# Kernel optimization log

Measured on AMD Instinct MI355X. Metric: run time of the kernel, lower is better.

## Reference

```python
import jax, jax.numpy as jnp
import numpy as np

N_NODES = 100000
N_HYPEREDGES = 20000
NNZ = 600000
D = 128


def setup_inputs() -> dict:
    key = jax.random.key(0)
    k = jax.random.split(key, 6)
    s = 1.0 / np.sqrt(D)
    x = jax.random.normal(k[0], (N_NODES, D), jnp.float32)
    node_idx = jax.random.randint(k[1], (NNZ,), 0, N_NODES, dtype=jnp.int64 if jax.config.jax_enable_x64 else jnp.int32)
    edge_idx = jax.random.randint(k[2], (NNZ,), 0, N_HYPEREDGES, dtype=jnp.int64 if jax.config.jax_enable_x64 else jnp.int32)
    conv_W = jax.random.uniform(k[3], (D, D), jnp.float32, -s, s)
    conv_b = jnp.zeros((D,), jnp.float32)
    res_W = jax.random.uniform(k[4], (D, D), jnp.float32, -s, s)
    res_b = jax.random.uniform(k[5], (D,), jnp.float32, -s, s)
    return {"x": x, "node_idx": node_idx, "edge_idx": edge_idx,
            "conv_W": conv_W, "conv_b": conv_b, "res_W": res_W, "res_b": res_b}


def hypergraph_conv(x, node_idx, edge_idx, W, b):
    # PyG HypergraphConv (no attention, unit hyperedge weights):
    #   out = D^{-1} H B^{-1} H^T (x W) + b
    y = x @ W                                                      # [N, D]
    ones = jnp.ones(node_idx.shape, dtype=y.dtype)
    deg_n = jax.ops.segment_sum(ones, node_idx, num_segments=N_NODES)        # node degree
    deg_e = jax.ops.segment_sum(ones, edge_idx, num_segments=N_HYPEREDGES)   # hyperedge size
    inv_n = jnp.where(deg_n > 0, 1.0 / deg_n, 0.0)
    inv_e = jnp.where(deg_e > 0, 1.0 / deg_e, 0.0)
    # node -> hyperedge aggregation, normalized by B^{-1}
    e_feat = jax.ops.segment_sum(y[node_idx], edge_idx, num_segments=N_HYPEREDGES)
    e_feat = e_feat * inv_e[:, None]                               # [E, D]
    # hyperedge -> node aggregation, normalized by D^{-1}
    out = jax.ops.segment_sum(e_feat[edge_idx], node_idx, num_segments=N_NODES)
    out = out * inv_n[:, None]                                     # [N, D]
    return out + b


def reference(x, node_idx, edge_idx, conv_W, conv_b, res_W, res_b):
    h = hypergraph_conv(x, node_idx, edge_idx, conv_W, conv_b)     # layer_num = 1
    return (x @ res_W + res_b) + h                                 # residual Linear + conv out
```

## Files before the change

kernel.cpp:

```cpp
#include <hip/hip_runtime.h>

#define N_NODES 100000
#define N_EDGES 20000
#define NNZ_C   600000
#define D 128

typedef short bf16x8 __attribute__((ext_vector_type(8)));
typedef float f32x4  __attribute__((ext_vector_type(4)));

__device__ __forceinline__ unsigned short f2bf(float f) {
    unsigned int u = __float_as_uint(f);
    u = (u + 0x7fffu + ((u >> 16) & 1u)) >> 16;
    return (unsigned short)u;
}
__device__ __forceinline__ float bf2f(unsigned short h) {
    return __uint_as_float((unsigned int)h << 16);
}
__device__ __forceinline__ unsigned int pk_trunc(float lo, float hi) {
    return __builtin_amdgcn_perm(__float_as_uint(hi), __float_as_uint(lo),
                                 0x07060302);
}

#define CH 4096
#define NCHUNK 147
#define CONVB 256
#define WBLK 8
#define EBW 16
#define NBE 1250
#define ECAP 768
#define NBW 64
#define NBN 1563
#define NCAP 640
#define PADI 32
#define GCUR_INTS ((NBE + NBN) * PADI)
#define TAGSH 21
#define PKMASK 0x1FFFFF

#define GT 64
#define XPAD 136

__global__ __launch_bounds__(512) void fused_bin_conv(
    const float* __restrict__ x,
    const int* __restrict__ nidx, const int* __restrict__ eidx,
    const float* __restrict__ cW, const float* __restrict__ rW,
    unsigned short* __restrict__ xb,
    unsigned short* __restrict__ wtc, unsigned short* __restrict__ wtr,
    int* __restrict__ bucket_e, int* __restrict__ bucket_n,
    int* __restrict__ gcur_e, int* __restrict__ gcur_n) {
    __shared__ int srt[CH];
    __shared__ int cnt[NBN], lbase[NBN], gbase[NBN], cur[NBN];
    const int bid = blockIdx.x;
    const int tid = threadIdx.x;

    if (bid >= NCHUNK + CONVB) {
        const int t0 = (bid - NCHUNK - CONVB) * 4096;
        for (int i = tid; i < 4096; i += 512) {
            const int t = t0 + i;
            const int m = t >> 14, idx = t & 16383;
            const int f = idx & 127, k = idx >> 7;
            const float* src = m ? rW : cW;
            unsigned short* dst = m ? wtr : wtc;
            dst[f * D + k] = f2bf(src[k * D + f]);
        }
        return;
    }
    if (bid >= NCHUNK) {
        const int total8 = N_NODES * D / 8;
        for (int g = (bid - NCHUNK) * 512 + tid; g < total8;
             g += CONVB * 512) {
            const float4 a = *(const float4*)(x + (size_t)g * 8);
            const float4 c = *(const float4*)(x + (size_t)g * 8 + 4);
            uint4 v;
            v.x = pk_trunc(a.x, a.y);
            v.y = pk_trunc(a.z, a.w);
            v.z = pk_trunc(c.x, c.y);
            v.w = pk_trunc(c.z, c.w);
            *(uint4*)(xb + (size_t)g * 8) = v;
        }
        return;
    }

    const int j0 = bid * CH;
    const int jn = (j0 + CH < NNZ_C) ? CH : NNZ_C - j0;
#pragma unroll
    for (int s = 0; s < 2; ++s) {
        const int nb = s ? NBN : NBE;
        int* gc = s ? gcur_n : gcur_e;
        int* dst = s ? bucket_n : bucket_e;
        const int cap = s ? NCAP : ECAP;
        for (int i = tid; i < nb; i += 512) cnt[i] = 0;
        __syncthreads();
        for (int i = tid; i < jn; i += 512) {
            const int id = s ? nidx[j0 + i] : eidx[j0 + i];
            atomicAdd(&cnt[s ? (id >> 6) : (id >> 4)], 1);
        }
        __syncthreads();
        if (tid < 64) {
            int loc[25];
            int ssum = 0;
            const int k0 = tid * 25;
#pragma unroll
            for (int k = 0; k < 25; ++k) {
                const int idx = k0 + k;
                loc[k] = ssum;
                if (idx < nb) ssum += cnt[idx];
            }
            int v = ssum;
#pragma unroll
            for (int off = 1; off < 64; off <<= 1) {
                const int t = __shfl_up(v, off);
                if (tid >= off) v += t;
            }
            const int base = v - ssum;
#pragma unroll
            for (int k = 0; k < 25; ++k) {
                const int idx = k0 + k;
                if (idx < nb) {
                    lbase[idx] = base + loc[k];
                    cur[idx] = base + loc[k];
                }
            }
        }
        __syncthreads();
        for (int i = tid; i < nb; i += 512)
            gbase[i] = cnt[i] ? atomicAdd(&gc[i * PADI], cnt[i]) : 0;
        __syncthreads();
        for (int i = tid; i < jn; i += 512) {
            const int e = eidx[j0 + i], n = nidx[j0 + i];
            const int b = s ? (n >> 6) : (e >> 4);
            const unsigned pk = s ? (unsigned)(((n & 63) << 15) | e)
                                  : (unsigned)(((e & 15) << 17) | n);
            const int pos = atomicAdd(&cur[b], 1);
            srt[pos] = (int)(pk | ((unsigned)b << TAGSH));
        }
        __syncthreads();
        for (int i = tid; i < jn; i += 512) {
            const unsigned v = (unsigned)srt[i];
            const int b = (int)(v >> TAGSH);
            const int o2 = gbase[b] + (i - lbase[b]);
            if (o2 < cap) dst[b * cap + o2] = (int)(v & PKMASK);
        }
        __syncthreads();
    }
}

__global__ __launch_bounds__(256) void edge_mean(
    const int* __restrict__ bucket_e, const int* __restrict__ gcur_e,
    const unsigned short* __restrict__ xb, unsigned short* __restrict__ sb) {
    __shared__ int srt[ECAP];
    __shared__ int cnt[EBW + 1];
    __shared__ int cur[EBW];
    const int tid = threadIdx.x;
    const int b = blockIdx.x;
    int W = gcur_e[b * PADI];
    if (W > ECAP) W = ECAP;
    if (tid <= EBW) cnt[tid] = 0;
    __syncthreads();
    const int* src = bucket_e + b * ECAP;
    for (int i = tid; i < W; i += 256)
        atomicAdd(&cnt[src[i] >> 17], 1);
    __syncthreads();
    if (tid < EBW) {
        const int c = cnt[tid];
        int v = c;
#pragma unroll
        for (int off = 1; off < EBW; off <<= 1) {
            const int t = __shfl_up(v, off);
            if (tid >= off) v += t;
        }
        cnt[tid] = v - c;
        cur[tid] = v - c;
        if (tid == EBW - 1) cnt[EBW] = v;
    }
    __syncthreads();
    for (int i = tid; i < W; i += 256) {
        const int p = src[i];
        const int pos = atomicAdd(&cur[p >> 17], 1);
        srt[pos] = p & 0x1FFFF;
    }
    __syncthreads();

    const int g = tid >> 4;
    const int l = tid & 15;
    const int beg = cnt[g], end = cnt[g + 1];
    float acc[8] = {};
    int j = beg;
    for (; j + 8 <= end; j += 8) {
        bf16x8 p[8];
#pragma unroll
        for (int q = 0; q < 8; ++q)
            p[q] = *(const bf16x8*)(xb + (size_t)srt[j + q] * D + l * 8);
#pragma unroll
        for (int i = 0; i < 8; ++i) {
            float t0 = bf2f((unsigned short)p[0][i]) + bf2f((unsigned short)p[1][i]);
            float t1 = bf2f((unsigned short)p[2][i]) + bf2f((unsigned short)p[3][i]);
            float t2 = bf2f((unsigned short)p[4][i]) + bf2f((unsigned short)p[5][i]);
            float t3 = bf2f((unsigned short)p[6][i]) + bf2f((unsigned short)p[7][i]);
            acc[i] += (t0 + t1) + (t2 + t3);
        }
    }
    for (; j + 4 <= end; j += 4) {
        const int n0 = srt[j], n1 = srt[j + 1];
        const int n2 = srt[j + 2], n3 = srt[j + 3];
        const bf16x8 p0 = *(const bf16x8*)(xb + (size_t)n0 * D + l * 8);
        const bf16x8 p1 = *(const bf16x8*)(xb + (size_t)n1 * D + l * 8);
        const bf16x8 p2 = *(const bf16x8*)(xb + (size_t)n2 * D + l * 8);
        const bf16x8 p3 = *(const bf16x8*)(xb + (size_t)n3 * D + l * 8);
#pragma unroll
        for (int i = 0; i < 8; ++i)
            acc[i] += (bf2f((unsigned short)p0[i]) + bf2f((unsigned short)p1[i]))
                    + (bf2f((unsigned short)p2[i]) + bf2f((unsigned short)p3[i]));
    }
    for (; j < end; ++j) {
        const bf16x8 p = *(const bf16x8*)(xb + (size_t)srt[j] * D + l * 8);
#pragma unroll
        for (int i = 0; i < 8; ++i) acc[i] += bf2f((unsigned short)p[i]);
    }
    const int deg = end - beg;
    const float inv = deg ? 1.f / (float)deg : 0.f;
    bf16x8 o;
#pragma unroll
    for (int i = 0; i < 8; ++i) o[i] = (short)f2bf(acc[i] * inv);
    *(bf16x8*)(sb + (size_t)(b * EBW + g) * D + l * 8) = o;
}

__global__ __launch_bounds__(512, 4) void node_gemm(
    const int* __restrict__ bucket_n, const int* __restrict__ gcur_n,
    const unsigned short* __restrict__ sb, const unsigned short* __restrict__ xb,
    const unsigned short* __restrict__ wtc, const unsigned short* __restrict__ wtr,
    const float* __restrict__ cbias, const float* __restrict__ rbias,
    float* __restrict__ out) {
    __shared__ int srt[NCAP];
    __shared__ int cnt[NBW + 1];
    __shared__ int cur[NBW];
    __shared__ unsigned short zs[NBW * XPAD];
    __shared__ unsigned short xs[GT * XPAD];
    const int tid = threadIdx.x;
    const int b = blockIdx.x;

    int W = gcur_n[b * PADI];
    if (W > NCAP) W = NCAP;
    if (tid <= NBW) cnt[tid] = 0;
    __syncthreads();
    const int* src = bucket_n + b * NCAP;
    for (int i = tid; i < W; i += 512)
        atomicAdd(&cnt[src[i] >> 15], 1);
    __syncthreads();
    if (tid < 64) {
        const int c = cnt[tid];
        int v = c;
#pragma unroll
        for (int off = 1; off < 64; off <<= 1) {
            const int t = __shfl_up(v, off);
            if (tid >= off) v += t;
        }
        cnt[tid] = v - c;
        cur[tid] = v - c;
        if (tid == 63) cnt[NBW] = v;
    }
    __syncthreads();
    for (int i = tid; i < W; i += 512) {
        const int p = src[i];
        const int pos = atomicAdd(&cur[p >> 15], 1);
        srt[pos] = p & 0x7FFF;
    }
    __syncthreads();

    {
        const int g = tid >> 4;
        const int l = tid & 15;
#pragma unroll
        for (int u = 0; u < 2; ++u) {
            const int nl = g * 2 + u;
            const int beg = cnt[nl], end = cnt[nl + 1];
            float acc[8] = {};
            int j = beg;
            for (; j + 4 <= end; j += 4) {
                const int e0 = srt[j], e1 = srt[j + 1];
                const int e2 = srt[j + 2], e3 = srt[j + 3];
                const bf16x8 p0 = *(const bf16x8*)(sb + (size_t)e0 * D + l * 8);
                const bf16x8 p1 = *(const bf16x8*)(sb + (size_t)e1 * D + l * 8);
                const bf16x8 p2 = *(const bf16x8*)(sb + (size_t)e2 * D + l * 8);
                const bf16x8 p3 = *(const bf16x8*)(sb + (size_t)e3 * D + l * 8);
#pragma unroll
                for (int i = 0; i < 8; ++i)
                    acc[i] += (bf2f((unsigned short)p0[i]) + bf2f((unsigned short)p1[i]))
                            + (bf2f((unsigned short)p2[i]) + bf2f((unsigned short)p3[i]));
            }
            for (; j < end; ++j) {
                const bf16x8 p = *(const bf16x8*)(sb + (size_t)srt[j] * D + l * 8);
#pragma unroll
                for (int i = 0; i < 8; ++i) acc[i] += bf2f((unsigned short)p[i]);
            }
            const int deg = end - beg;
            const float inv = deg ? 1.f / (float)deg : 0.f;
            bf16x8 o;
#pragma unroll
            for (int i = 0; i < 8; ++i) o[i] = (short)f2bf(acc[i] * inv);
            *(bf16x8*)(zs + nl * XPAD + l * 8) = o;
        }
    }

    const int w    = tid >> 6;
    const int lane = tid & 63;
    const int quad = lane >> 4;
    const int l16  = lane & 15;
    const int f0   = w * 16;
    const int f    = f0 + l16;
    bf16x8 Ac[4], Ar[4];
#pragma unroll
    for (int kc = 0; kc < 4; ++kc) {
        Ac[kc] = *(const bf16x8*)(wtc + (size_t)f * D + kc * 32 + quad * 8);
        Ar[kc] = *(const bf16x8*)(wtr + (size_t)f * D + kc * 32 + quad * 8);
    }
    const float4 cb4 = *(const float4*)(cbias + f0 + quad * 4);
    const float4 rb4 = *(const float4*)(rbias + f0 + quad * 4);
    const float4 bias = {cb4.x + rb4.x, cb4.y + rb4.y,
                         cb4.z + rb4.z, cb4.w + rb4.w};

    {
        const int r0 = tid >> 3;
        const int qp = tid & 7;
        int n = b * NBW + r0;
        if (n >= N_NODES) n = N_NODES - 1;
        const uint4* sx = (const uint4*)(xb + (size_t)n * D + qp * 16);
        uint4* dx = (uint4*)(xs + r0 * XPAD + qp * 16);
        dx[0] = sx[0]; dx[1] = sx[1];
    }
    __syncthreads();
    f32x4 acc[4] = {};
#pragma unroll
    for (int g = 0; g < 4; ++g)
#pragma unroll
        for (int kc = 0; kc < 4; ++kc) {
            const int ro = (g * 16 + l16) * XPAD + kc * 32 + quad * 8;
            const bf16x8 Bz = *(const bf16x8*)(zs + ro);
            const bf16x8 Bx = *(const bf16x8*)(xs + ro);
            acc[g] = __builtin_amdgcn_mfma_f32_16x16x32_bf16(Ac[kc], Bz, acc[g], 0, 0, 0);
            acc[g] = __builtin_amdgcn_mfma_f32_16x16x32_bf16(Ar[kc], Bx, acc[g], 0, 0, 0);
        }
#pragma unroll
    for (int g = 0; g < 4; ++g) {
        const int n = b * NBW + g * 16 + l16;
        if (n >= N_NODES) continue;
        float4 o;
        o.x = acc[g][0] + bias.x;
        o.y = acc[g][1] + bias.y;
        o.z = acc[g][2] + bias.z;
        o.w = acc[g][3] + bias.w;
        *(float4*)(out + (size_t)n * D + f0 + quad * 4) = o;
    }
}

extern "C" void kernel_launch(void* const* d_in, const int* in_sizes, int n_in,
                              void* d_out, int out_size, void* d_ws,
                              size_t ws_size, hipStream_t stream) {
    const float* x  = (const float*)d_in[0];
    const int* nidx = (const int*)d_in[1];
    const int* eidx = (const int*)d_in[2];
    const float* cW = (const float*)d_in[3];
    const float* cb = (const float*)d_in[4];
    const float* rW = (const float*)d_in[5];
    const float* rb = (const float*)d_in[6];
    float* out = (float*)d_out;

    char* ws = (char*)d_ws;
    size_t off = 0;
    auto alloc = [&](size_t bytes) {
        size_t o = off;
        off += (bytes + 255) & ~(size_t)255;
        return o;
    };
    unsigned short* xb  = (unsigned short*)(ws + alloc((size_t)N_NODES * D * 2));
    unsigned short* sb  = (unsigned short*)(ws + alloc((size_t)N_EDGES * D * 2));
    unsigned short* wtc = (unsigned short*)(ws + alloc((size_t)D * D * 2));
    unsigned short* wtr = (unsigned short*)(ws + alloc((size_t)D * D * 2));
    int* bucket_e = (int*)(ws + alloc((size_t)NBE * ECAP * 4));
    int* bucket_n = (int*)(ws + alloc((size_t)NBN * NCAP * 4));
    int* gcur     = (int*)(ws + alloc((size_t)GCUR_INTS * 4));
    int* gcur_e = gcur;
    int* gcur_n = gcur + NBE * PADI;

    hipMemsetAsync(gcur, 0, (size_t)GCUR_INTS * 4, stream);

    fused_bin_conv<<<NCHUNK + CONVB + WBLK, 512, 0, stream>>>(
        x, nidx, eidx, cW, rW, xb, wtc, wtr,
        bucket_e, bucket_n, gcur_e, gcur_n);

    edge_mean<<<NBE, 256, 0, stream>>>(bucket_e, gcur_e, xb, sb);
    node_gemm<<<NBN, 512, 0, stream>>>(bucket_n, gcur_n, sb, xb,
                                       wtc, wtr, cb, rb, out);
}
```

Baseline: 192.5 us.

## Shard global bucket cursors to spread atomic contention across shards

Each bin now has 16 shard slots, chosen by block index, each with its own padded cursor and a small fixed capacity. The binning blocks spread their global atomicAdds over these shard counters instead of one counter per bin. edge_mean and node_gemm then walk all 16 shard segments to gather entries. The cost is a 16x larger cursor array to memset, 16 separate cursor reads and short serial loops in each consumer block, and a chance of dropping entries if one shard overflows its small capacity.

After: 224.5 us. 16.6% more time.

```diff
diff --git a/kernel.cpp b/kernel.cpp
--- a/kernel.cpp
+++ b/kernel.cpp
@@ -25,14 +25,15 @@
 #define NCHUNK 147
 #define CONVB 256
 #define WBLK 8
+#define NSH 16
 #define EBW 16
 #define NBE 1250
-#define ECAP 768
+#define ECAP_SH 96
 #define NBW 64
 #define NBN 1563
-#define NCAP 640
+#define NCAP_SH 64
 #define PADI 32
-#define GCUR_INTS ((NBE + NBN) * PADI)
+#define GCUR_INTS ((NBE + NBN) * NSH * PADI)
 #define TAGSH 21
 #define PKMASK 0x1FFFFF
 
@@ -80,6 +81,7 @@
         return;
     }
 
+    const int shard = bid & (NSH - 1);
     const int j0 = bid * CH;
     const int jn = (j0 + CH < NNZ_C) ? CH : NNZ_C - j0;
 #pragma unroll
@@ -87,7 +89,7 @@
         const int nb = s ? NBN : NBE;
         int* gc = s ? gcur_n : gcur_e;
         int* dst = s ? bucket_n : bucket_e;
-        const int cap = s ? NCAP : ECAP;
+        const int capsh = s ? NCAP_SH : ECAP_SH;
         for (int i = tid; i < nb; i += 512) cnt[i] = 0;
         __syncthreads();
         for (int i = tid; i < jn; i += 512) {
@@ -123,7 +125,7 @@
         }
         __syncthreads();
         for (int i = tid; i < nb; i += 512)
-            gbase[i] = cnt[i] ? atomicAdd(&gc[i * PADI], cnt[i]) : 0;
+            gbase[i] = cnt[i] ? atomicAdd(&gc[(i * NSH + shard) * PADI], cnt[i]) : 0;
         __syncthreads();
         for (int i = tid; i < jn; i += 512) {
             const int e = eidx[j0 + i], n = nidx[j0 + i];
@@ -138,7 +140,8 @@
             const unsigned v = (unsigned)srt[i];
             const int b = (int)(v >> TAGSH);
             const int o2 = gbase[b] + (i - lbase[b]);
-            if (o2 < cap) dst[b * cap + o2] = (int)(v & PKMASK);
+            if (o2 < capsh)
+                dst[(b * NSH + shard) * capsh + o2] = (int)(v & PKMASK);
         }
         __syncthreads();
     }
@@ -147,18 +150,25 @@
 __global__ __launch_bounds__(256) void edge_mean(
     const int* __restrict__ bucket_e, const int* __restrict__ gcur_e,
     const unsigned short* __restrict__ xb, unsigned short* __restrict__ sb) {
-    __shared__ int srt[ECAP];
+    __shared__ int srt[NSH * ECAP_SH];
     __shared__ int cnt[EBW + 1];
     __shared__ int cur[EBW];
     const int tid = threadIdx.x;
     const int b = blockIdx.x;
-    int W = gcur_e[b * PADI];
-    if (W > ECAP) W = ECAP;
+    int Wsh[NSH];
+#pragma unroll
+    for (int sh = 0; sh < NSH; ++sh) {
+        int c = gcur_e[(b * NSH + sh) * PADI];
+        Wsh[sh] = (c < ECAP_SH) ? c : ECAP_SH;
+    }
     if (tid <= EBW) cnt[tid] = 0;
     __syncthreads();
-    const int* src = bucket_e + b * ECAP;
-    for (int i = tid; i < W; i += 256)
-        atomicAdd(&cnt[src[i] >> 17], 1);
+#pragma unroll
+    for (int sh = 0; sh < NSH; ++sh) {
+        const int* seg = bucket_e + (b * NSH + sh) * ECAP_SH;
+        for (int i = tid; i < Wsh[sh]; i += 256)
+            atomicAdd(&cnt[seg[i] >> 17], 1);
+    }
     __syncthreads();
     if (tid < EBW) {
         const int c = cnt[tid];
@@ -173,10 +183,14 @@
         if (tid == EBW - 1) cnt[EBW] = v;
     }
     __syncthreads();
-    for (int i = tid; i < W; i += 256) {
-        const int p = src[i];
-        const int pos = atomicAdd(&cur[p >> 17], 1);
-        srt[pos] = p & 0x1FFFF;
+#pragma unroll
+    for (int sh = 0; sh < NSH; ++sh) {
+        const int* seg = bucket_e + (b * NSH + sh) * ECAP_SH;
+        for (int i = tid; i < Wsh[sh]; i += 256) {
+            const int p = seg[i];
+            const int pos = atomicAdd(&cur[p >> 17], 1);
+            srt[pos] = p & 0x1FFFF;
+        }
     }
     __syncthreads();
 
@@ -230,7 +244,7 @@
     const unsigned short* __restrict__ wtc, const unsigned short* __restrict__ wtr,
     const float* __restrict__ cbias, const float* __restrict__ rbias,
     float* __restrict__ out) {
-    __shared__ int srt[NCAP];
+    __shared__ int srt[NSH * NCAP_SH];
     __shared__ int cnt[NBW + 1];
     __shared__ int cur[NBW];
     __shared__ unsigned short zs[NBW * XPAD];
@@ -238,13 +252,20 @@
     const int tid = threadIdx.x;
     const int b = blockIdx.x;
 
-    int W = gcur_n[b * PADI];
-    if (W > NCAP) W = NCAP;
+    int Wsh[NSH];
+#pragma unroll
+    for (int sh = 0; sh < NSH; ++sh) {
+        int c = gcur_n[(b * NSH + sh) * PADI];
+        Wsh[sh] = (c < NCAP_SH) ? c : NCAP_SH;
+    }
     if (tid <= NBW) cnt[tid] = 0;
     __syncthreads();
-    const int* src = bucket_n + b * NCAP;
-    for (int i = tid; i < W; i += 512)
-        atomicAdd(&cnt[src[i] >> 15], 1);
+#pragma unroll
+    for (int sh = 0; sh < NSH; ++sh) {
+        const int* seg = bucket_n + (b * NSH + sh) * NCAP_SH;
+        for (int i = tid; i < Wsh[sh]; i += 512)
+            atomicAdd(&cnt[seg[i] >> 15], 1);
+    }
     __syncthreads();
     if (tid < 64) {
         const int c = cnt[tid];
@@ -259,10 +280,14 @@
         if (tid == 63) cnt[NBW] = v;
     }
     __syncthreads();
-    for (int i = tid; i < W; i += 512) {
-        const int p = src[i];
-        const int pos = atomicAdd(&cur[p >> 15], 1);
-        srt[pos] = p & 0x7FFF;
+#pragma unroll
+    for (int sh = 0; sh < NSH; ++sh) {
+        const int* seg = bucket_n + (b * NSH + sh) * NCAP_SH;
+        for (int i = tid; i < Wsh[sh]; i += 512) {
+            const int p = seg[i];
+            const int pos = atomicAdd(&cur[p >> 15], 1);
+            srt[pos] = p & 0x7FFF;
+        }
     }
     __syncthreads();
 
@@ -375,11 +400,11 @@
     unsigned short* sb  = (unsigned short*)(ws + alloc((size_t)N_EDGES * D * 2));
     unsigned short* wtc = (unsigned short*)(ws + alloc((size_t)D * D * 2));
     unsigned short* wtr = (unsigned short*)(ws + alloc((size_t)D * D * 2));
-    int* bucket_e = (int*)(ws + alloc((size_t)NBE * ECAP * 4));
-    int* bucket_n = (int*)(ws + alloc((size_t)NBN * NCAP * 4));
+    int* bucket_e = (int*)(ws + alloc((size_t)NBE * NSH * ECAP_SH * 4));
+    int* bucket_n = (int*)(ws + alloc((size_t)NBN * NSH * NCAP_SH * 4));
     int* gcur     = (int*)(ws + alloc((size_t)GCUR_INTS * 4));
     int* gcur_e = gcur;
-    int* gcur_n = gcur + NBE * PADI;
+    int* gcur_n = gcur + NBE * NSH * PADI;
 
     hipMemsetAsync(gcur, 0, (size_t)GCUR_INTS * 4, stream);
 
```
